# Kernel optimization log

Measured on AMD Instinct MI355X. Metric: run time of the kernel, lower is better.

## Reference

```python
import jax, jax.numpy as jnp
import numpy as np

B, D_MODEL, H = 2048, 1024, 16
D_K = D_MODEL // H


def setup_inputs() -> dict:
    root = jax.random.key(0)
    ks = jax.random.split(root, 11)
    w_scale = 1.0 / np.sqrt(D_MODEL).astype(np.float32)
    inp = {
        "query": jax.random.normal(ks[0], (B, D_MODEL), jnp.float32),
        "key": jax.random.normal(ks[1], (B, D_MODEL), jnp.float32),
        "value": jax.random.normal(ks[2], (B, D_MODEL), jnp.float32),
        # Linear weights (used as x @ W + b)
        "Wq": jax.random.normal(ks[3], (D_MODEL, D_MODEL), jnp.float32) * w_scale,
        "bq": jnp.zeros((D_MODEL,), jnp.float32),
        "Wk": jax.random.normal(ks[4], (D_MODEL, D_MODEL), jnp.float32) * w_scale,
        "bk": jnp.zeros((D_MODEL,), jnp.float32),
        "Wv": jax.random.normal(ks[5], (D_MODEL, D_MODEL), jnp.float32) * w_scale,
        "bv": jnp.zeros((D_MODEL,), jnp.float32),
        # Random U drawn fresh each forward in torch; materialized here for determinism.
        # torch shape: randn(d_model, nbatches*d_k).view(nbatches, h, d_k, d_k)
        "U": jax.random.normal(ks[6], (B, H, D_K, D_K), jnp.float32),
    }
    return inp


def reference(query, key, value, Wq, bq, Wk, bk, Wv, bv, U):
    b, dm = query.shape
    h = U.shape[1]
    dk = dm // h
    residual = key
    # QKV projections, then view(b, -1, h, dk).transpose(1, 2) -> [b, h, 1, dk]
    q = (query @ Wq + bq).reshape(b, 1, h, dk).transpose(0, 2, 1, 3)
    k = (key @ Wk + bk).reshape(b, 1, h, dk).transpose(0, 2, 1, 3)
    v = (value @ Wv + bv).reshape(b, 1, h, dk).transpose(0, 2, 1, 3)
    # attn_weight = (q @ U) @ k^T : [b,h,1,dk] @ [b,h,dk,dk] @ [b,h,dk,1] -> [b,h,1,1]
    aw = jnp.matmul(q, U)
    scores = jnp.matmul(aw, jnp.swapaxes(k, -1, -2))
    p = jax.nn.softmax(scores, axis=-1)  # dropout is identity at inference
    # context = p^T @ v : [b,h,1,1] @ [b,h,1,dk] -> [b,h,1,dk]
    ctx = jnp.matmul(jnp.swapaxes(p, -1, -2), v)
    ctx = jnp.swapaxes(ctx, 1, 2).reshape(b, dm)
    return ctx + residual
```

## Files before the change

### kernel.cpp

```cpp
#include <hip/hip_runtime.h>
#include <hip/hip_bf16.h>


#define M_DIM 2048
#define N_DIM 1024
#define K_DIM 1024

typedef __attribute__((ext_vector_type(8))) short short8;
typedef __attribute__((ext_vector_type(4))) float f32x4;

__device__ inline unsigned rne_bf16(float f) {
    unsigned u = __builtin_bit_cast(unsigned, f);
    return (u + 0x7FFFu + ((u >> 16) & 1u)) >> 16;
}
__device__ inline unsigned pack2(float lo, float hi) {
    return rne_bf16(lo) | (rne_bf16(hi) << 16);
}

__global__ __launch_bounds__(256)
void convert_kernel(const float* __restrict__ value, const float* __restrict__ Wv,
                    short* __restrict__ Vb, short* __restrict__ WvTb) {
    __shared__ unsigned tr[64 * 36];
    const int b = blockIdx.x, tid = threadIdx.x;
    if (b < 1024) {
        int g = b * 256 + tid;
        int row = g >> 7, ch = g & 127;
        int kt = ch >> 3, c = ch & 7;
        int tm = row >> 6, r = row & 63;
        const float* p = value + (size_t)row * K_DIM + ch * 8;
        f32x4 a0 = *(const f32x4*)p;
        f32x4 a1 = *(const f32x4*)(p + 4);
        union { short8 s; unsigned u[4]; } o;
        o.u[0] = pack2(a0[0], a0[1]);
        o.u[1] = pack2(a0[2], a0[3]);
        o.u[2] = pack2(a1[0], a1[1]);
        o.u[3] = pack2(a1[2], a1[3]);
        *(short8*)&Vb[(size_t)(tm * 16 + kt) * 4096 + r * 64 + ((c ^ (r & 7)) << 3)] = o.s;
    } else {
        int b2 = b - 1024;
        int tn = b2 & 15, kt = b2 >> 4;
        #pragma unroll
        for (int s = 0; s < 2; ++s) {
            int kp = (tid >> 4) + s * 16;
            int n4 = (tid & 15) * 4;
            const float* bp = Wv + (size_t)(kt * 64 + 2 * kp) * N_DIM + tn * 64 + n4;
            f32x4 b0 = *(const f32x4*)bp;
            f32x4 b1 = *(const f32x4*)(bp + N_DIM);
            #pragma unroll
            for (int m = 0; m < 4; ++m)
                tr[(n4 + m) * 36 + kp] = pack2(b0[m], b1[m]);
        }
        __syncthreads();
        int n = tid >> 2;
        #pragma unroll
        for (int h = 0; h < 2; ++h) {
            int c = (tid & 3) + 4 * h;
            union { short8 s; unsigned u[4]; } o;
            #pragma unroll
            for (int p = 0; p < 4; ++p)
                o.u[p] = tr[n * 36 + c * 4 + p];
            *(short8*)&WvTb[(size_t)(tn * 16 + kt) * 4096 + n * 64 + ((c ^ (n & 7)) << 3)] = o.s;
        }
    }
}

__device__ inline void gl_lds16(const short* g, short* l) {
    __builtin_amdgcn_global_load_lds((const __attribute__((address_space(1))) void*)g,
                                     (__attribute__((address_space(3))) void*)l,
                                     16, 0, 0);
}

__global__ __launch_bounds__(256)
void gemm_kernel(const short* __restrict__ Vb, const short* __restrict__ WvTb,
                 const float* __restrict__ key, const float* __restrict__ bv,
                 float* __restrict__ out) {
    __shared__ __align__(16) short As[4][4096];
    __shared__ __align__(16) short Bs[4][4096];

    const int tid = threadIdx.x;
    const int bid = blockIdx.x;
    const int swz = ((bid & 7) << 6) | (bid >> 3);
    const int bm = swz >> 4;
    const int bn = swz & 15;
    const int lane = tid & 63;
    const int wid = tid >> 6;
    const int wr = wid >> 1;
    const int wc = wid & 1;

    const short* Abase = Vb + (size_t)bm * 16 * 4096;
    const short* Bbase = WvTb + (size_t)bn * 16 * 4096;
    const int row0 = bm * 64, col0 = bn * 64;

    const int colA = col0 + wc * 32 + (lane & 15);
    const int rbaseA = row0 + wr * 32 + ((lane >> 4) * 4);
    float keyr[2][2][4];
    float bvr[2];
    #pragma unroll
    for (int fn = 0; fn < 2; ++fn) bvr[fn] = bv[colA + fn * 16];
    #pragma unroll
    for (int fm = 0; fm < 2; ++fm)
        #pragma unroll
        for (int fn = 0; fn < 2; ++fn)
            #pragma unroll
            for (int i = 0; i < 4; ++i)
                keyr[fm][fn][i] = key[(size_t)(rbaseA + fm * 16 + i) * N_DIM + colA + fn * 16];

    f32x4 acc[2][2] = {};

    auto stage = [&](int buf, int kt) {
        const short* ga = Abase + (size_t)kt * 4096 + tid * 8;
        const short* gb = Bbase + (size_t)kt * 4096 + tid * 8;
        gl_lds16(ga,        &As[buf][tid * 8]);
        gl_lds16(ga + 2048, &As[buf][2048 + tid * 8]);
        gl_lds16(gb,        &Bs[buf][tid * 8]);
        gl_lds16(gb + 2048, &Bs[buf][2048 + tid * 8]);
    };

    auto compute = [&](int buf) {
        #pragma unroll
        for (int ks = 0; ks < 2; ++ks) {
            short8 afr[2], bfr[2];
            const int g = ks * 4 + (lane >> 4);
            #pragma unroll
            for (int fm = 0; fm < 2; ++fm) {
                int r = wr * 32 + fm * 16 + (lane & 15);
                afr[fm] = *(const short8*)&As[buf][r * 64 + ((g ^ (r & 7)) << 3)];
            }
            #pragma unroll
            for (int fn = 0; fn < 2; ++fn) {
                int n = wc * 32 + fn * 16 + (lane & 15);
                bfr[fn] = *(const short8*)&Bs[buf][n * 64 + ((g ^ (n & 7)) << 3)];
            }
            #pragma unroll
            for (int fm = 0; fm < 2; ++fm)
                #pragma unroll
                for (int fn = 0; fn < 2; ++fn)
                    acc[fm][fn] = __builtin_amdgcn_mfma_f32_16x16x32_bf16(
                        afr[fm], bfr[fn], acc[fm][fn], 0, 0, 0);
        }
    };

    stage(0, 0);
    stage(1, 1);
    stage(2, 2);

    #pragma unroll
    for (int kt = 0; kt < 16; ++kt) {
        if (kt <= 13)      asm volatile("s_waitcnt vmcnt(8)" ::: "memory");
        else if (kt == 14) asm volatile("s_waitcnt vmcnt(4)" ::: "memory");
        else               asm volatile("s_waitcnt vmcnt(0)" ::: "memory");
        __builtin_amdgcn_s_barrier();
        if (kt + 3 < 16) stage((kt + 3) & 3, kt + 3);
        compute(kt & 3);
    }

    #pragma unroll
    for (int fm = 0; fm < 2; ++fm) {
        #pragma unroll
        for (int fn = 0; fn < 2; ++fn) {
            int col = colA + fn * 16;
            #pragma unroll
            for (int i = 0; i < 4; ++i) {
                int r = rbaseA + fm * 16 + i;
                out[(size_t)r * N_DIM + col] = acc[fm][fn][i] + bvr[fn] + keyr[fm][fn][i];
            }
        }
    }
}

extern "C" void kernel_launch(void* const* d_in, const int* in_sizes, int n_in,
                              void* d_out, int out_size, void* d_ws, size_t ws_size,
                              hipStream_t stream) {
    const float* key   = (const float*)d_in[1];
    const float* value = (const float*)d_in[2];
    const float* Wv    = (const float*)d_in[7];
    const float* bv    = (const float*)d_in[8];
    float* out = (float*)d_out;

    short* Vb   = (short*)d_ws;
    short* WvTb = (short*)d_ws + (size_t)M_DIM * K_DIM;

    convert_kernel<<<1024 + 256, 256, 0, stream>>>(value, Wv, Vb, WvTb);
    gemm_kernel<<<512, 256, 0, stream>>>(Vb, WvTb, key, bv, out);
}
```

Before: 23.74 us.

## Enlarge GEMM block tile to 128x64 and halve grid size

```diff
diff --git a/kernel.cpp b/kernel.cpp
--- a/kernel.cpp
+++ b/kernel.cpp
@@ -15,6 +15,11 @@
 }
 __device__ inline unsigned pack2(float lo, float hi) {
     return rne_bf16(lo) | (rne_bf16(hi) << 16);
+}
+__device__ inline void gl_lds16(const short* g, short* l) {
+    __builtin_amdgcn_global_load_lds((const __attribute__((address_space(1))) void*)g,
+                                     (__attribute__((address_space(3))) void*)l,
+                                     16, 0, 0);
 }
 
 __global__ __launch_bounds__(256)
@@ -64,67 +69,65 @@
     }
 }
 
-__device__ inline void gl_lds16(const short* g, short* l) {
-    __builtin_amdgcn_global_load_lds((const __attribute__((address_space(1))) void*)g,
-                                     (__attribute__((address_space(3))) void*)l,
-                                     16, 0, 0);
-}
-
 __global__ __launch_bounds__(256)
 void gemm_kernel(const short* __restrict__ Vb, const short* __restrict__ WvTb,
                  const float* __restrict__ key, const float* __restrict__ bv,
                  float* __restrict__ out) {
-    __shared__ __align__(16) short As[4][4096];
+    __shared__ __align__(16) short As[4][8192];
     __shared__ __align__(16) short Bs[4][4096];
 
     const int tid = threadIdx.x;
     const int bid = blockIdx.x;
-    const int swz = ((bid & 7) << 6) | (bid >> 3);
-    const int bm = swz >> 4;
-    const int bn = swz & 15;
+    const int xcd = bid & 7, idx = bid >> 3;
+    const int bm2 = xcd * 2 + (idx >> 4);
+    const int bn  = idx & 15;
     const int lane = tid & 63;
     const int wid = tid >> 6;
     const int wr = wid >> 1;
     const int wc = wid & 1;
 
-    const short* Abase = Vb + (size_t)bm * 16 * 4096;
-    const short* Bbase = WvTb + (size_t)bn * 16 * 4096;
-    const int row0 = bm * 64, col0 = bn * 64;
+    const short* Ab0 = Vb + (size_t)(bm2 * 2) * 16 * 4096;
+    const short* Ab1 = Vb + (size_t)(bm2 * 2 + 1) * 16 * 4096;
+    const short* Bb  = WvTb + (size_t)bn * 16 * 4096;
+    const int row0 = bm2 * 128, col0 = bn * 64;
 
     const int colA = col0 + wc * 32 + (lane & 15);
-    const int rbaseA = row0 + wr * 32 + ((lane >> 4) * 4);
-    float keyr[2][2][4];
+    const int rbaseA = row0 + wr * 64 + ((lane >> 4) * 4);
+    float keyr[4][2][4];
     float bvr[2];
     #pragma unroll
     for (int fn = 0; fn < 2; ++fn) bvr[fn] = bv[colA + fn * 16];
     #pragma unroll
-    for (int fm = 0; fm < 2; ++fm)
+    for (int fm = 0; fm < 4; ++fm)
         #pragma unroll
         for (int fn = 0; fn < 2; ++fn)
             #pragma unroll
             for (int i = 0; i < 4; ++i)
                 keyr[fm][fn][i] = key[(size_t)(rbaseA + fm * 16 + i) * N_DIM + colA + fn * 16];
 
-    f32x4 acc[2][2] = {};
+    f32x4 acc[4][2] = {};
 
     auto stage = [&](int buf, int kt) {
-        const short* ga = Abase + (size_t)kt * 4096 + tid * 8;
-        const short* gb = Bbase + (size_t)kt * 4096 + tid * 8;
-        gl_lds16(ga,        &As[buf][tid * 8]);
-        gl_lds16(ga + 2048, &As[buf][2048 + tid * 8]);
-        gl_lds16(gb,        &Bs[buf][tid * 8]);
-        gl_lds16(gb + 2048, &Bs[buf][2048 + tid * 8]);
+        const short* ga0 = Ab0 + (size_t)kt * 4096 + tid * 8;
+        const short* ga1 = Ab1 + (size_t)kt * 4096 + tid * 8;
+        const short* gb  = Bb  + (size_t)kt * 4096 + tid * 8;
+        gl_lds16(ga0,        &As[buf][tid * 8]);
+        gl_lds16(ga0 + 2048, &As[buf][2048 + tid * 8]);
+        gl_lds16(ga1,        &As[buf][4096 + tid * 8]);
+        gl_lds16(ga1 + 2048, &As[buf][6144 + tid * 8]);
+        gl_lds16(gb,         &Bs[buf][tid * 8]);
+        gl_lds16(gb + 2048,  &Bs[buf][2048 + tid * 8]);
     };
 
     auto compute = [&](int buf) {
         #pragma unroll
         for (int ks = 0; ks < 2; ++ks) {
-            short8 afr[2], bfr[2];
+            short8 afr[4], bfr[2];
             const int g = ks * 4 + (lane >> 4);
             #pragma unroll
-            for (int fm = 0; fm < 2; ++fm) {
-                int r = wr * 32 + fm * 16 + (lane & 15);
-                afr[fm] = *(const short8*)&As[buf][r * 64 + ((g ^ (r & 7)) << 3)];
+            for (int fm = 0; fm < 4; ++fm) {
+                int r = fm * 16 + (lane & 15);
+                afr[fm] = *(const short8*)&As[buf][wr * 4096 + r * 64 + ((g ^ (r & 7)) << 3)];
             }
             #pragma unroll
             for (int fn = 0; fn < 2; ++fn) {
@@ -132,7 +135,7 @@
                 bfr[fn] = *(const short8*)&Bs[buf][n * 64 + ((g ^ (n & 7)) << 3)];
             }
             #pragma unroll
-            for (int fm = 0; fm < 2; ++fm)
+            for (int fm = 0; fm < 4; ++fm)
                 #pragma unroll
                 for (int fn = 0; fn < 2; ++fn)
                     acc[fm][fn] = __builtin_amdgcn_mfma_f32_16x16x32_bf16(
@@ -146,8 +149,8 @@
 
     #pragma unroll
     for (int kt = 0; kt < 16; ++kt) {
-        if (kt <= 13)      asm volatile("s_waitcnt vmcnt(8)" ::: "memory");
-        else if (kt == 14) asm volatile("s_waitcnt vmcnt(4)" ::: "memory");
+        if (kt <= 13)      asm volatile("s_waitcnt vmcnt(12)" ::: "memory");
+        else if (kt == 14) asm volatile("s_waitcnt vmcnt(6)" ::: "memory");
         else               asm volatile("s_waitcnt vmcnt(0)" ::: "memory");
         __builtin_amdgcn_s_barrier();
         if (kt + 3 < 16) stage((kt + 3) & 3, kt + 3);
@@ -155,7 +158,7 @@
     }
 
     #pragma unroll
-    for (int fm = 0; fm < 2; ++fm) {
+    for (int fm = 0; fm < 4; ++fm)
         #pragma unroll
         for (int fn = 0; fn < 2; ++fn) {
             int col = colA + fn * 16;
@@ -165,7 +168,6 @@
                 out[(size_t)r * N_DIM + col] = acc[fm][fn][i] + bvr[fn] + keyr[fm][fn][i];
             }
         }
-    }
 }
 
 extern "C" void kernel_launch(void* const* d_in, const int* in_sizes, int n_in,
@@ -181,5 +183,5 @@
     short* WvTb = (short*)d_ws + (size_t)M_DIM * K_DIM;
 
     convert_kernel<<<1024 + 256, 256, 0, stream>>>(value, Wv, Vb, WvTb);
-    gemm_kernel<<<512, 256, 0, stream>>>(Vb, WvTb, key, bv, out);
+    gemm_kernel<<<256, 256, 0, stream>>>(Vb, WvTb, key, bv, out);
 }
```

Result: slower. 26.53 us (+11.8%).

## Use 128x64 GEMM tiles with 512 threads and an LDS-staged vectorized epilogue

Applied to the files above, without the earlier changes.

```diff
diff --git a/kernel.cpp b/kernel.cpp
--- a/kernel.cpp
+++ b/kernel.cpp
@@ -15,6 +15,11 @@
 }
 __device__ inline unsigned pack2(float lo, float hi) {
     return rne_bf16(lo) | (rne_bf16(hi) << 16);
+}
+__device__ inline void gl_lds16(const short* g, short* l) {
+    __builtin_amdgcn_global_load_lds((const __attribute__((address_space(1))) void*)g,
+                                     (__attribute__((address_space(3))) void*)l,
+                                     16, 0, 0);
 }
 
 __global__ __launch_bounds__(256)
@@ -64,56 +69,34 @@
     }
 }
 
-__device__ inline void gl_lds16(const short* g, short* l) {
-    __builtin_amdgcn_global_load_lds((const __attribute__((address_space(1))) void*)g,
-                                     (__attribute__((address_space(3))) void*)l,
-                                     16, 0, 0);
-}
-
-__global__ __launch_bounds__(256)
+__global__ __launch_bounds__(512)
 void gemm_kernel(const short* __restrict__ Vb, const short* __restrict__ WvTb,
                  const float* __restrict__ key, const float* __restrict__ bv,
                  float* __restrict__ out) {
-    __shared__ __align__(16) short As[4][4096];
+    __shared__ __align__(16) short As[4][8192];
     __shared__ __align__(16) short Bs[4][4096];
 
     const int tid = threadIdx.x;
     const int bid = blockIdx.x;
-    const int swz = ((bid & 7) << 6) | (bid >> 3);
-    const int bm = swz >> 4;
-    const int bn = swz & 15;
+    const int xcd = bid & 7, idx = bid >> 3;
+    const int bm2 = xcd * 2 + (idx >> 4);
+    const int bn  = idx & 15;
     const int lane = tid & 63;
     const int wid = tid >> 6;
     const int wr = wid >> 1;
     const int wc = wid & 1;
 
-    const short* Abase = Vb + (size_t)bm * 16 * 4096;
-    const short* Bbase = WvTb + (size_t)bn * 16 * 4096;
-    const int row0 = bm * 64, col0 = bn * 64;
-
-    const int colA = col0 + wc * 32 + (lane & 15);
-    const int rbaseA = row0 + wr * 32 + ((lane >> 4) * 4);
-    float keyr[2][2][4];
-    float bvr[2];
-    #pragma unroll
-    for (int fn = 0; fn < 2; ++fn) bvr[fn] = bv[colA + fn * 16];
-    #pragma unroll
-    for (int fm = 0; fm < 2; ++fm)
-        #pragma unroll
-        for (int fn = 0; fn < 2; ++fn)
-            #pragma unroll
-            for (int i = 0; i < 4; ++i)
-                keyr[fm][fn][i] = key[(size_t)(rbaseA + fm * 16 + i) * N_DIM + colA + fn * 16];
+    const short* Ab0 = Vb + (size_t)(bm2 * 2) * 16 * 4096;
+    const short* Ab1 = Vb + (size_t)(bm2 * 2 + 1) * 16 * 4096;
+    const short* Bb  = WvTb + (size_t)bn * 16 * 4096;
+    const int row0 = bm2 * 128, col0 = bn * 64;
 
     f32x4 acc[2][2] = {};
 
     auto stage = [&](int buf, int kt) {
-        const short* ga = Abase + (size_t)kt * 4096 + tid * 8;
-        const short* gb = Bbase + (size_t)kt * 4096 + tid * 8;
-        gl_lds16(ga,        &As[buf][tid * 8]);
-        gl_lds16(ga + 2048, &As[buf][2048 + tid * 8]);
-        gl_lds16(gb,        &Bs[buf][tid * 8]);
-        gl_lds16(gb + 2048, &Bs[buf][2048 + tid * 8]);
+        gl_lds16(Ab0 + (size_t)kt * 4096 + tid * 8, &As[buf][tid * 8]);
+        gl_lds16(Ab1 + (size_t)kt * 4096 + tid * 8, &As[buf][4096 + tid * 8]);
+        gl_lds16(Bb  + (size_t)kt * 4096 + tid * 8, &Bs[buf][tid * 8]);
     };
 
     auto compute = [&](int buf) {
@@ -146,25 +129,38 @@
 
     #pragma unroll
     for (int kt = 0; kt < 16; ++kt) {
-        if (kt <= 13)      asm volatile("s_waitcnt vmcnt(8)" ::: "memory");
-        else if (kt == 14) asm volatile("s_waitcnt vmcnt(4)" ::: "memory");
+        if (kt <= 13)      asm volatile("s_waitcnt vmcnt(6)" ::: "memory");
+        else if (kt == 14) asm volatile("s_waitcnt vmcnt(3)" ::: "memory");
         else               asm volatile("s_waitcnt vmcnt(0)" ::: "memory");
         __builtin_amdgcn_s_barrier();
         if (kt + 3 < 16) stage((kt + 3) & 3, kt + 3);
         compute(kt & 3);
     }
 
+    __syncthreads();
+    float* T = (float*)&As[0][0];
     #pragma unroll
-    for (int fm = 0; fm < 2; ++fm) {
+    for (int fm = 0; fm < 2; ++fm)
         #pragma unroll
         for (int fn = 0; fn < 2; ++fn) {
-            int col = colA + fn * 16;
+            int c = wc * 32 + fn * 16 + (lane & 15);
             #pragma unroll
             for (int i = 0; i < 4; ++i) {
-                int r = rbaseA + fm * 16 + i;
-                out[(size_t)r * N_DIM + col] = acc[fm][fn][i] + bvr[fn] + keyr[fm][fn][i];
+                int r = wr * 32 + fm * 16 + (lane >> 4) * 4 + i;
+                T[r * 68 + c] = acc[fm][fn][i];
             }
         }
+    __syncthreads();
+    #pragma unroll
+    for (int it = 0; it < 4; ++it) {
+        int r = it * 32 + (tid >> 4);
+        int q = tid & 15;
+        f32x4 vv = *(f32x4*)&T[r * 68 + q * 4];
+        int grow = row0 + r, gcol = col0 + q * 4;
+        f32x4 kv = *(const f32x4*)&key[(size_t)grow * N_DIM + gcol];
+        f32x4 bb = *(const f32x4*)&bv[gcol];
+        vv = vv + kv + bb;
+        *(f32x4*)&out[(size_t)grow * N_DIM + gcol] = vv;
     }
 }
 
@@ -181,5 +177,5 @@
     short* WvTb = (short*)d_ws + (size_t)M_DIM * K_DIM;
 
     convert_kernel<<<1024 + 256, 256, 0, stream>>>(value, Wv, Vb, WvTb);
-    gemm_kernel<<<512, 256, 0, stream>>>(Vb, WvTb, key, bv, out);
+    gemm_kernel<<<256, 512, 0, stream>>>(Vb, WvTb, key, bv, out);
 }
```

New measurement: 22.33 us. -5.9%, faster.
